# Optimization experiments

Hardware: AMD Instinct MI355X
Metric: run time of the kernel (lower is better)

Reference implementation:

```python
import jax, jax.numpy as jnp
import numpy as np
import math

B, T, D, H, DM = 2, 2048, 1024, 16, 256
DK = D // H

def setup_inputs() -> dict:
    key = jax.random.key(0)
    ks = jax.random.split(key, 13)
    s = 0.02
    return {
        "Hx": jax.random.normal(ks[0], (B, D, T, 1), jnp.float32),
        "Hf": jax.random.normal(ks[1], (B, T, D), jnp.float32),
        "Gm": jax.random.normal(ks[2], (B, T, DM), jnp.float32),
        "Wg": jax.random.normal(ks[3], (T, DM), jnp.float32) * s,
        "bg": jax.random.normal(ks[4], (T,), jnp.float32) * s,
        "Wq": jax.random.normal(ks[5], (D, 2 * D), jnp.float32) * s,
        "bq": jax.random.normal(ks[6], (D,), jnp.float32) * s,
        "Wk": jax.random.normal(ks[7], (D, 2 * D), jnp.float32) * s,
        "bk": jax.random.normal(ks[8], (D,), jnp.float32) * s,
        "Wv": jax.random.normal(ks[9], (D, D), jnp.float32) * s,
        "bv": jax.random.normal(ks[10], (D,), jnp.float32) * s,
        "Wo": jax.random.normal(ks[11], (D, D), jnp.float32) * s,
        "bo": jax.random.normal(ks[12], (D,), jnp.float32) * s,
    }

def reference(Hx, Hf, Gm, Wg, bg, Wq, bq, Wk, bk, Wv, bv, Wo, bo):
    # Hx: (B, D, T, 1) -> (B, T, D)
    hx = jnp.transpose(Hx[..., 0], (0, 2, 1))
    h_cat = jnp.concatenate([hx, Hf], axis=-1)          # (B, T, 2D)
    Q = h_cat @ Wq.T + bq                               # (B, T, D)
    K = h_cat @ Wk.T + bk
    V = hx @ Wv.T + bv
    # split heads: (B, H, T, DK)
    Q = Q.reshape(B, T, H, DK).transpose(0, 2, 1, 3)
    K = K.reshape(B, T, H, DK).transpose(0, 2, 1, 3)
    V = V.reshape(B, T, H, DK).transpose(0, 2, 1, 3)
    scores = jnp.einsum('bhqd,bhkd->bhqk', Q, K) / math.sqrt(DK)
    bias = Gm @ Wg.T + bg                                # (B, T, T)
    scores = scores + bias[:, None, :, :]
    attn = jax.nn.softmax(scores, axis=-1)
    out = jnp.einsum('bhqk,bhkd->bhqd', attn, V)
    out = out.transpose(0, 2, 1, 3).reshape(B, T, D)
    return out @ Wo.T + bo
```

## Files before the change

kernel.cpp:

```cpp
#include <hip/hip_runtime.h>
#include <hip/hip_bf16.h>

using bf16 = __hip_bfloat16;
typedef __attribute__((ext_vector_type(8))) __bf16 bf16x8;
typedef __attribute__((ext_vector_type(4))) float f32x4;

#define GLB_AS(p) ((const __attribute__((address_space(1))) unsigned int*)(p))
#define LDS_AS(p) ((__attribute__((address_space(3))) unsigned int*)(p))

__device__ __forceinline__ void async_copy16(const void* g, void* l) {
  __builtin_amdgcn_global_load_lds(GLB_AS(g), LDS_AS(l), 16, 0, 0);
}

__device__ __forceinline__ f32x4 mfma16x16x32(bf16x8 a, bf16x8 b, f32x4 c) {
  return __builtin_amdgcn_mfma_f32_16x16x32_bf16(a, b, c, 0, 0, 0);
}

__device__ __forceinline__ float bfu2f(unsigned short u) {
  union { unsigned int i; float f; } x;
  x.i = (unsigned int)u << 16;
  return x.f;
}

#define LOG2E 1.44269504f

__global__ __launch_bounds__(256) void pack_hx(const float* __restrict__ Hx,
                                               bf16* __restrict__ hcat) {
  __shared__ float tile[64][65];
  const int t0 = blockIdx.x * 64, d0 = blockIdx.y * 64, b = blockIdx.z;
  const int c = threadIdx.x & 63, r0 = threadIdx.x >> 6;
#pragma unroll
  for (int i = 0; i < 16; ++i) {
    const int rd = r0 + i * 4;
    tile[rd][c] = Hx[((size_t)(b * 1024 + d0 + rd)) * 2048 + t0 + c];
  }
  __syncthreads();
#pragma unroll
  for (int i = 0; i < 16; ++i) {
    const int ct = r0 + i * 4;
    hcat[((size_t)(b * 2048 + t0 + ct)) * 2048 + d0 + c] =
        __float2bfloat16(tile[c][ct]);
  }
}

__global__ __launch_bounds__(256) void pack_all(
    const float* __restrict__ Hf, const float* __restrict__ Wq,
    const float* __restrict__ Wk, const float* __restrict__ Wv,
    const float* __restrict__ Wo, const float* __restrict__ Wg,
    const float* __restrict__ Gm, const float* __restrict__ bq,
    const float* __restrict__ bk, const float* __restrict__ bv,
    bf16* __restrict__ hcat, bf16* __restrict__ Wqkvb, bf16* __restrict__ Wob,
    bf16* __restrict__ Wgb, bf16* __restrict__ Gmb,
    float* __restrict__ qkvbias) {
  const int gid = blockIdx.x * 256 + threadIdx.x;
  const float* src = nullptr;
  bf16* dst = nullptr;
  int lg = 0, ldo = 0, off = 0, idx = 0;
  bool zero = false;
  if (gid < 1048576) { idx = gid; src = Hf; dst = hcat; lg = 8; ldo = 2048; off = 1024; }
  else if (gid < 1572864) { idx = gid - 1048576; src = Wq; dst = Wqkvb; lg = 9; ldo = 2048; }
  else if (gid < 2097152) { idx = gid - 1572864; src = Wk; dst = Wqkvb + (size_t)1024 * 2048; lg = 9; ldo = 2048; }
  else if (gid < 2359296) { idx = gid - 2097152; src = Wv; dst = Wqkvb + (size_t)2048 * 2048; lg = 8; ldo = 2048; }
  else if (gid < 2621440) { idx = gid - 2359296; zero = true; dst = Wqkvb + (size_t)2048 * 2048 + 1024; lg = 8; ldo = 2048; }
  else if (gid < 2883584) { idx = gid - 2621440; src = Wo; dst = Wob; lg = 8; ldo = 1024; }
  else if (gid < 3014656) { idx = gid - 2883584; src = Wg; dst = Wgb; lg = 6; ldo = 256; }
  else if (gid < 3276800) { idx = gid - 3014656; src = Gm; dst = Gmb; lg = 6; ldo = 256; }
  else if (gid < 3277056) { const int i = gid - 3276800; ((float4*)qkvbias)[i] = ((const float4*)bq)[i]; return; }
  else if (gid < 3277312) { const int i = gid - 3277056; ((float4*)(qkvbias + 1024))[i] = ((const float4*)bk)[i]; return; }
  else { const int i = gid - 3277312; ((float4*)(qkvbias + 2048))[i] = ((const float4*)bv)[i]; return; }
  const int row = idx >> lg, c = idx & ((1 << lg) - 1);
  bf16* o = dst + (size_t)row * ldo + off + c * 4;
  __align__(8) bf16 tmp[4];
  if (zero) {
    tmp[0] = tmp[1] = tmp[2] = tmp[3] = __float2bfloat16(0.f);
  } else {
    const float4 v = ((const float4*)src)[(size_t)idx];
    tmp[0] = __float2bfloat16(v.x); tmp[1] = __float2bfloat16(v.y);
    tmp[2] = __float2bfloat16(v.z); tmp[3] = __float2bfloat16(v.w);
  }
  *(ushort4*)o = *(const ushort4*)tmp;
}

__global__ __launch_bounds__(512, 2) void gemm_qkv_bias(
    const bf16* __restrict__ hcat, const bf16* __restrict__ Wqkv,
    const float* __restrict__ qkvbias, const bf16* __restrict__ Gmb,
    const bf16* __restrict__ Wgb, const float* __restrict__ bg,
    bf16* __restrict__ QKb, bf16* __restrict__ Vt, bf16* __restrict__ biasS) {
  __shared__ __align__(16) bf16 AS[2][256][64];
  __shared__ __align__(16) bf16 BS[2][256][64];
  const int lin = blockIdx.x;
  const bool isqkv = lin < 192;
  int m0, n0, Kd, KT, nit2;
  const bf16 *Ag, *Bg;
  const float* biasv;
  if (isqkv) {
    const int xcd = lin & 7, kk = lin >> 3;
    const int mloc = kk / 6, nloc = kk - mloc * 6;
    m0 = ((xcd >> 1) * 4 + mloc) * 256;
    n0 = ((xcd & 1) * 6 + nloc) * 256;
    Ag = hcat; Bg = Wqkv; biasv = qkvbias;
    Kd = 2048; KT = 32; nit2 = 16;
  } else {
    const int l2 = lin - 192;
    m0 = (l2 >> 3) * 256;
    n0 = (l2 & 7) * 256;
    Ag = Gmb; Bg = Wgb; biasv = bg;
    Kd = 256; KT = 4; nit2 = 2;
  }
  const int tid = threadIdx.x, lane = tid & 63, w = tid >> 6;
  const int w8 = w * 8, ln3 = lane >> 3, ch = lane & 7;
  const int fr = lane & 15, ck = lane >> 4;
  const int wm64 = (w >> 2) * 64;
  const int wn32 = (w & 3) * 32;

  f32x4 acc[8][4];
  const f32x4 fzero = {0.f, 0.f, 0.f, 0.f};
#pragma unroll
  for (int i = 0; i < 8; ++i)
#pragma unroll
    for (int j = 0; j < 4; ++j) acc[i][j] = fzero;

  auto stageA = [&](int buf, int mh, int kt) {
    const int k0 = kt * 64;
#pragma unroll
    for (int l = 0; l < 2; ++l) {
      const int rit = mh * 128 + l * 64 + w8 + ln3;
      async_copy16(Ag + (size_t)(m0 + rit) * Kd + k0 + ((ch ^ ln3) << 3),
                   (char*)&AS[buf][0][0] + ((mh * 128 + l * 64 + w8) << 7));
    }
  };
  auto stageB = [&](int buf, int nh, int kt) {
    const int k0 = kt * 64;
#pragma unroll
    for (int l = 0; l < 2; ++l) {
      const int rit = nh * 128 + l * 64 + w8 + ln3;
      async_copy16(Bg + (size_t)(n0 + rit) * Kd + k0 + ((ch ^ ln3) << 3),
                   (char*)&BS[buf][0][0] + ((nh * 128 + l * 64 + w8) << 7));
    }
  };

  bf16x8 af[4][2], bA[2][2], bB[2][2];
  auto ldA = [&](int buf, int mh) {
#pragma unroll
    for (int i = 0; i < 4; ++i)
#pragma unroll
      for (int ks = 0; ks < 2; ++ks)
        af[i][ks] = *(const bf16x8*)(
            &AS[buf][mh * 128 + wm64 + i * 16 + fr][0] +
            (((ks * 4 + ck) ^ (fr & 7)) << 3));
  };
  auto ldB = [&](bf16x8 (&dst)[2][2], int buf, int nh) {
#pragma unroll
    for (int j = 0; j < 2; ++j)
#pragma unroll
      for (int ks = 0; ks < 2; ++ks)
        dst[j][ks] = *(const bf16x8*)(
            &BS[buf][nh * 128 + wn32 + j * 16 + fr][0] +
            (((ks * 4 + ck) ^ (fr & 7)) << 3));
  };

#define BAR() __builtin_amdgcn_s_barrier()
#define LGKM0() asm volatile("s_waitcnt lgkmcnt(0)" ::: "memory")
#define MMAQ(MH, NH, BF)                                                      \
  __builtin_amdgcn_s_setprio(1);                                              \
  _Pragma("unroll") for (int i_ = 0; i_ < 4; ++i_) {                          \
    _Pragma("unroll") for (int j_ = 0; j_ < 2; ++j_) {                        \
      acc[(MH) * 4 + i_][(NH) * 2 + j_] = mfma16x16x32(                       \
          af[i_][0], BF[j_][0], acc[(MH) * 4 + i_][(NH) * 2 + j_]);           \
      acc[(MH) * 4 + i_][(NH) * 2 + j_] = mfma16x16x32(                       \
          af[i_][1], BF[j_][1], acc[(MH) * 4 + i_][(NH) * 2 + j_]);           \
    }                                                                         \
  }                                                                           \
  __builtin_amdgcn_s_setprio(0);

  stageA(0, 0, 0); stageB(0, 0, 0); stageB(0, 1, 0); stageA(0, 1, 0);
  stageA(1, 0, 1); stageB(1, 0, 1);
  asm volatile("s_waitcnt vmcnt(4)" ::: "memory");
  BAR();

  for (int it = 0; it < nit2; ++it) {
    const int kodd = 2 * it + 1;
    const int kn0 = (2 * it + 2 < KT) ? 2 * it + 2 : KT - 1;
    const int kn1 = (2 * it + 3 < KT) ? 2 * it + 3 : KT - 1;

    ldA(0, 0); ldB(bA, 0, 0);
    stageB(1, 1, kodd);
    asm volatile("s_waitcnt lgkmcnt(8)");
    BAR(); LGKM0();
    MMAQ(0, 0, bA);
    BAR();
    ldB(bB, 0, 1);
    stageA(1, 1, kodd);
    BAR(); LGKM0();
    MMAQ(0, 1, bB);
    BAR();
    ldA(0, 1);
    stageA(0, 0, kn0);
    BAR(); LGKM0();
    MMAQ(1, 0, bA);
    BAR();
    stageB(0, 0, kn0);
    asm volatile("s_waitcnt vmcnt(4)" ::: "memory");
    BAR();
    MMAQ(1, 1, bB);
    BAR();
    ldA(1, 0); ldB(bA, 1, 0);
    stageB(0, 1, kn0);
    asm volatile("s_waitcnt lgkmcnt(8)");
    BAR(); LGKM0();
    MMAQ(0, 0, bA);
    BAR();
    ldB(bB, 1, 1);
    stageA(0, 1, kn0);
    BAR(); LGKM0();
    MMAQ(0, 1, bB);
    BAR();
    ldA(1, 1);
    stageA(1, 0, kn1);
    BAR(); LGKM0();
    MMAQ(1, 0, bA);
    BAR();
    stageB(1, 0, kn1);
    asm volatile("s_waitcnt vmcnt(4)" ::: "memory");
    BAR();
    MMAQ(1, 1, bB);
    BAR();
  }
  asm volatile("s_waitcnt vmcnt(0)" ::: "memory");

  const int erow = (lane >> 4) * 4, ecol = lane & 15;
  if (!isqkv) {
#pragma unroll
    for (int ai = 0; ai < 8; ++ai) {
      const int gm0 = m0 + (ai >> 2) * 128 + wm64 + (ai & 3) * 16 + erow;
#pragma unroll
      for (int bj = 0; bj < 4; ++bj) {
        const int gn = n0 + (bj >> 1) * 128 + wn32 + (bj & 1) * 16 + ecol;
        const float bv = biasv[gn];
#pragma unroll
        for (int r = 0; r < 4; ++r)
          biasS[(size_t)(gm0 + r) * 2048 + gn] =
              __float2bfloat16((acc[ai][bj][r] + bv) * LOG2E);
      }
    }
  } else if (n0 < 2048) {
    const float sc = (n0 < 1024) ? 0.125f * LOG2E : 1.0f;
#pragma unroll
    for (int ai = 0; ai < 8; ++ai) {
      const int gm0 = m0 + (ai >> 2) * 128 + wm64 + (ai & 3) * 16 + erow;
#pragma unroll
      for (int bj = 0; bj < 4; ++bj) {
        const int gn = n0 + (bj >> 1) * 128 + wn32 + (bj & 1) * 16 + ecol;
        const float bv = biasv[gn];
#pragma unroll
        for (int r = 0; r < 4; ++r)
          QKb[(size_t)(gm0 + r) * 2048 + gn] =
              __float2bfloat16((acc[ai][bj][r] + bv) * sc);
      }
    }
  } else {
#pragma unroll
    for (int ai = 0; ai < 8; ++ai) {
      const int gm0 = m0 + (ai >> 2) * 128 + wm64 + (ai & 3) * 16 + erow;
      const int bb = gm0 >> 11;
      const int t = gm0 & 2047;
#pragma unroll
      for (int bj = 0; bj < 4; ++bj) {
        const int gn = n0 + (bj >> 1) * 128 + wn32 + (bj & 1) * 16 + ecol;
        const float bv = biasv[gn];
        const int d = gn - 2048;
        __align__(8) bf16 tmp[4];
#pragma unroll
        for (int r = 0; r < 4; ++r)
          tmp[r] = __float2bfloat16(acc[ai][bj][r] + bv);
        *(ushort4*)(Vt + ((size_t)(bb * 1024 + d)) * 2048 + t) =
            *(const ushort4*)tmp;
      }
    }
  }
#undef MMAQ
#undef LGKM0
#undef BAR
}

__global__ __launch_bounds__(256) void gemm_out(const bf16* __restrict__ A,
                                                const bf16* __restrict__ W,
                                                const float* __restrict__ biasv,
                                                float* __restrict__ C) {
  __shared__ __align__(16) bf16 As[2][128 * 64];
  __shared__ __align__(16) bf16 Bs[2][64 * 64];
  const int lin = blockIdx.x;
  const int xcd = lin & 7;
  const int kk = lin >> 3;
  const int m0 = (kk >> 1) * 128;
  const int n0 = (xcd * 2 + (kk & 1)) * 64;
  const int tid = threadIdx.x, lane = tid & 63, w = tid >> 6;
  const int wm = (w >> 1) * 64, wn = (w & 1) * 32;
  const int fr = lane & 15;
  const int ck = lane >> 4;

  f32x4 acc[4][2];
  const f32x4 fzero = {0.f, 0.f, 0.f, 0.f};
#pragma unroll
  for (int i = 0; i < 4; ++i)
#pragma unroll
    for (int j = 0; j < 2; ++j) acc[i][j] = fzero;

  auto stage = [&](int it, int buf) {
    const int k0 = it * 64;
#pragma unroll
    for (int is = 0; is < 4; ++is) {
      const int off = is * 4096 + w * 1024;
      const int row = (off >> 7) + (lane >> 3);
      const int sch = ((lane & 7) ^ (row & 7)) * 8;
      async_copy16(A + (size_t)(m0 + row) * 1024 + k0 + sch,
                   (char*)As[buf] + off);
      if (is < 2)
        async_copy16(W + (size_t)(n0 + row) * 1024 + k0 + sch,
                     (char*)Bs[buf] + off);
    }
  };

  stage(0, 0);
  __syncthreads();
  for (int it = 0; it < 16; ++it) {
    const int cur = it & 1;
    if (it + 1 < 16) stage(it + 1, cur ^ 1);
#pragma unroll
    for (int ks = 0; ks < 2; ++ks) {
      bf16x8 af[4], bfr[2];
      const int swk0 = (((ks * 4 + ck) ^ (fr & 7))) * 8;
#pragma unroll
      for (int i = 0; i < 4; ++i)
        af[i] = *(const bf16x8*)(As[cur] + (wm + i * 16 + fr) * 64 + swk0);
#pragma unroll
      for (int j = 0; j < 2; ++j)
        bfr[j] = *(const bf16x8*)(Bs[cur] + (wn + j * 16 + fr) * 64 + swk0);
#pragma unroll
      for (int i = 0; i < 4; ++i)
#pragma unroll
        for (int j = 0; j < 2; ++j)
          acc[i][j] = mfma16x16x32(af[i], bfr[j], acc[i][j]);
    }
    __syncthreads();
  }
  const int erow = (lane >> 4) * 4;
  const int ecol = lane & 15;
#pragma unroll
  for (int i = 0; i < 4; ++i) {
    const int gm0 = m0 + wm + i * 16 + erow;
#pragma unroll
    for (int j = 0; j < 2; ++j) {
      const int gn = n0 + wn + j * 16 + ecol;
      const float bv = biasv[gn];
#pragma unroll
      for (int r = 0; r < 4; ++r)
        C[(size_t)(gm0 + r) * 1024 + gn] = acc[i][j][r] + bv;
    }
  }
}

__global__ __launch_bounds__(256) void flash_attn(
    const bf16* __restrict__ Qm, const bf16* __restrict__ Km,
    const bf16* __restrict__ Vtm, const bf16* __restrict__ biasS,
    float* __restrict__ Op0, float* __restrict__ Op1,
    float* __restrict__ lpart) {
  __shared__ __align__(16) bf16 Ks[2][64 * 64];
  __shared__ __align__(16) bf16 Vs[2][64 * 64];
  __shared__ __align__(16) bf16 Ps[4 * 32 * 72];
  const int lin = blockIdx.x;
  const int xcd = lin & 7;
  const int kk = lin >> 3;
  const int cl = kk & 1;
  const int r2 = kk >> 1;
  const int half = r2 & 1;
  const int q0 = (r2 >> 1) * 128;
  const int combo = xcd * 2 + cl;
  const int hp = combo & 7;
  const int b = combo >> 3;
  const int tid = threadIdx.x, lane = tid & 63, w = tid >> 6;
  const int ql = lane & 15, qk = lane >> 4;
  const int T = 2048, D = 1024;
  const int sw0 = (qk ^ (ql & 7)) * 8;
  const int sw1 = ((qk + 4) ^ (ql & 7)) * 8;

  bf16x8 qf[2][2][2];
#pragma unroll
  for (int hh = 0; hh < 2; ++hh)
#pragma unroll
    for (int qt = 0; qt < 2; ++qt)
#pragma unroll
      for (int ks = 0; ks < 2; ++ks)
        qf[hh][qt][ks] = *(const bf16x8*)(
            Qm + (size_t)(b * T + q0 + w * 32 + qt * 16 + ql) * 2048 +
            (hp * 2 + hh) * 64 + ks * 32 + qk * 8);

  f32x4 acc[2][4][2];
  const f32x4 fzero = {0.f, 0.f, 0.f, 0.f};
#pragma unroll
  for (int hh = 0; hh < 2; ++hh)
#pragma unroll
    for (int dt = 0; dt < 4; ++dt)
#pragma unroll
      for (int qt = 0; qt < 2; ++qt) acc[hh][dt][qt] = fzero;
  float lp[2][2] = {{0.f, 0.f}, {0.f, 0.f}};

  const bf16* kbase0 = Km + (size_t)(b * T) * 2048 + (hp * 2) * 64;
  const bf16* vbase0 = Vtm + (size_t)(b * D + hp * 2 * 64) * 2048;
  const bf16* bb0 = biasS + (size_t)(b * T + q0 + w * 32 + ql) * 2048 + qk * 4;
  bf16* pb = Ps + w * 2304;

  for (int j = 0; j < 16; ++j) {
    const int jj = half * 16 + j;
    __syncthreads();
#pragma unroll
    for (int hh = 0; hh < 2; ++hh)
#pragma unroll
      for (int is = 0; is < 2; ++is) {
        const int off = is * 4096 + w * 1024;
        const int row = (off >> 7) + (lane >> 3);
        const int sch = ((lane & 7) ^ (row & 7)) * 8;
        async_copy16(kbase0 + (size_t)(jj * 64 + row) * 2048 + hh * 64 + sch,
                     (char*)Ks[hh] + off);
        async_copy16(vbase0 + (size_t)(hh * 64 + row) * 2048 + jj * 64 + sch,
                     (char*)Vs[hh] + off);
      }
    ushort4 bq[2][4];
#pragma unroll
    for (int qt = 0; qt < 2; ++qt)
#pragma unroll
      for (int jt = 0; jt < 4; ++jt)
        bq[qt][jt] = *(const ushort4*)(bb0 + (size_t)qt * 16 * 2048 + jj * 64 +
                                       jt * 16);
    __syncthreads();
#pragma unroll
    for (int hh = 0; hh < 2; ++hh) {
      const bf16* ksp = Ks[hh];
      const bf16* vsp = Vs[hh];
#pragma unroll
      for (int jt = 0; jt < 4; ++jt) {
        const bf16x8 kf0 = *(const bf16x8*)(ksp + (jt * 16 + ql) * 64 + sw0);
        const bf16x8 kf1 = *(const bf16x8*)(ksp + (jt * 16 + ql) * 64 + sw1);
#pragma unroll
        for (int qt = 0; qt < 2; ++qt) {
          f32x4 c;
          c[0] = bfu2f(bq[qt][jt].x); c[1] = bfu2f(bq[qt][jt].y);
          c[2] = bfu2f(bq[qt][jt].z); c[3] = bfu2f(bq[qt][jt].w);
          c = mfma16x16x32(kf0, qf[hh][qt][0], c);
          c = mfma16x16x32(kf1, qf[hh][qt][1], c);
          __align__(8) bf16 t4[4];
#pragma unroll
          for (int r = 0; r < 4; ++r) {
            const float pv = __builtin_amdgcn_exp2f(c[r]);
            lp[hh][qt] += pv;
            t4[r] = __float2bfloat16(pv);
          }
          *(ushort4*)(pb + (qt * 16 + ql) * 72 + jt * 16 + qk * 4) =
              *(const ushort4*)t4;
        }
      }
#pragma unroll
      for (int ks = 0; ks < 2; ++ks) {
        const bf16x8 pf0 = *(const bf16x8*)(pb + ql * 72 + ks * 32 + qk * 8);
        const bf16x8 pf1 =
            *(const bf16x8*)(pb + (16 + ql) * 72 + ks * 32 + qk * 8);
        const int sw = ks ? sw1 : sw0;
#pragma unroll
        for (int dt = 0; dt < 4; ++dt) {
          const bf16x8 vf = *(const bf16x8*)(vsp + (dt * 16 + ql) * 64 + sw);
          acc[hh][dt][0] = mfma16x16x32(pf0, vf, acc[hh][dt][0]);
          acc[hh][dt][1] = mfma16x16x32(pf1, vf, acc[hh][dt][1]);
        }
      }
    }
  }
#pragma unroll
  for (int hh = 0; hh < 2; ++hh)
#pragma unroll
    for (int qt = 0; qt < 2; ++qt) {
      lp[hh][qt] += __shfl_xor(lp[hh][qt], 16);
      lp[hh][qt] += __shfl_xor(lp[hh][qt], 32);
    }
  if (qk == 0) {
#pragma unroll
    for (int hh = 0; hh < 2; ++hh)
#pragma unroll
      for (int qt = 0; qt < 2; ++qt)
        lpart[half * 65536 + (b * 16 + hp * 2 + hh) * 2048 + q0 + w * 32 +
              qt * 16 + ql] = lp[hh][qt];
  }
  float* Op = half ? Op1 : Op0;
#pragma unroll
  for (int hh = 0; hh < 2; ++hh)
#pragma unroll
    for (int qt = 0; qt < 2; ++qt)
#pragma unroll
      for (int r = 0; r < 4; ++r) {
        const size_t orow =
            (size_t)(b * T + q0 + w * 32 + qt * 16 + qk * 4 + r);
#pragma unroll
        for (int dt = 0; dt < 4; ++dt)
          Op[orow * 1024 + (hp * 2 + hh) * 64 + dt * 16 + ql] =
              acc[hh][dt][qt][r];
      }
}

__global__ __launch_bounds__(256) void combine(const float* __restrict__ O0,
                                               const float* __restrict__ O1,
                                               const float* __restrict__ lpart,
                                               bf16* __restrict__ AOut) {
  const int idx = blockIdx.x * 256 + threadIdx.x;
  const int row = idx >> 8;
  const int col = (idx & 255) * 4;
  const int b = row >> 11, q = row & 2047, h = col >> 6;
  const int li = (b * 16 + h) * 2048 + q;
  const float inv = __builtin_amdgcn_rcpf(lpart[li] + lpart[65536 + li]);
  const float4 a = *(const float4*)(O0 + (size_t)row * 1024 + col);
  const float4 c = *(const float4*)(O1 + (size_t)row * 1024 + col);
  __align__(8) bf16 t[4] = {
      __float2bfloat16((a.x + c.x) * inv), __float2bfloat16((a.y + c.y) * inv),
      __float2bfloat16((a.z + c.z) * inv), __float2bfloat16((a.w + c.w) * inv)};
  *(ushort4*)(AOut + (size_t)row * 1024 + col) = *(const ushort4*)t;
}

extern "C" void kernel_launch(void* const* d_in, const int* in_sizes, int n_in,
                              void* d_out, int out_size, void* d_ws,
                              size_t ws_size, hipStream_t stream) {
  (void)in_sizes; (void)n_in; (void)out_size; (void)ws_size;
  const float* Hx = (const float*)d_in[0];
  const float* Hf = (const float*)d_in[1];
  const float* Gm = (const float*)d_in[2];
  const float* Wg = (const float*)d_in[3];
  const float* bg = (const float*)d_in[4];
  const float* Wq = (const float*)d_in[5];
  const float* bq = (const float*)d_in[6];
  const float* Wk = (const float*)d_in[7];
  const float* bk = (const float*)d_in[8];
  const float* Wv = (const float*)d_in[9];
  const float* bv = (const float*)d_in[10];
  const float* Wo = (const float*)d_in[11];
  const float* bo = (const float*)d_in[12];
  float* out = (float*)d_out;

  char* p = (char*)d_ws;
  bf16* hcat = (bf16*)p;   p += (size_t)4096 * 2048 * 2;
  bf16* QKb = (bf16*)p;    p += (size_t)4096 * 2048 * 2;
  bf16* Vtb = (bf16*)p;    p += (size_t)4096 * 1024 * 2;
  bf16* biasS = (bf16*)p;  p += (size_t)4096 * 2048 * 2;
  bf16* AOut = (bf16*)p;   p += (size_t)4096 * 1024 * 2;
  bf16* Wqkvb = (bf16*)p;  p += (size_t)3072 * 2048 * 2;
  bf16* Wob = (bf16*)p;    p += (size_t)1024 * 1024 * 2;
  bf16* Wgb = (bf16*)p;    p += (size_t)2048 * 256 * 2;
  bf16* Gmb = (bf16*)p;    p += (size_t)4096 * 256 * 2;
  float* qkvbias = (float*)p; p += (size_t)3072 * 4;
  float* Op1 = (float*)p;  p += (size_t)4096 * 1024 * 4;
  float* lpart = (float*)p; p += (size_t)2 * 65536 * 4;
  float* Op0 = (float*)hcat;

  pack_hx<<<dim3(32, 16, 2), 256, 0, stream>>>(Hx, hcat);
  pack_all<<<dim3(12803), 256, 0, stream>>>(Hf, Wq, Wk, Wv, Wo, Wg, Gm, bq, bk,
                                            bv, hcat, Wqkvb, Wob, Wgb, Gmb,
                                            qkvbias);
  gemm_qkv_bias<<<dim3(320), 512, 0, stream>>>(hcat, Wqkvb, qkvbias, Gmb,
                                               Wgb, bg, QKb, Vtb, biasS);
  flash_attn<<<dim3(512), 256, 0, stream>>>(QKb, QKb + 1024, Vtb, biasS,
                                            Op0, Op1, lpart);
  combine<<<dim3(4096), 256, 0, stream>>>(Op0, Op1, lpart, AOut);
  gemm_out<<<dim3(512), 256, 0, stream>>>(AOut, Wob, bo, out);
}
```

Baseline: 278.2 us.

## Double-buffer K/V tiles and prefetch bias one iteration ahead in attention

Result: slower. 346.3 us (+24.5%).

```diff
diff --git a/kernel.cpp b/kernel.cpp
--- a/kernel.cpp
+++ b/kernel.cpp
@@ -383,6 +383,8 @@
   const int T = 2048, D = 1024;
   const int sw0 = (qk ^ (ql & 7)) * 8;
   const int sw1 = ((qk + 4) ^ (ql & 7)) * 8;
+  const int ln3 = lane >> 3;
+  const int sch = ((lane & 7) ^ ln3) << 3;
 
   bf16x8 qf[2][2][2];
 #pragma unroll
@@ -410,70 +412,110 @@
   const bf16* bb0 = biasS + (size_t)(b * T + q0 + w * 32 + ql) * 2048 + qk * 4;
   bf16* pb = Ps + w * 2304;
 
-  for (int j = 0; j < 16; ++j) {
-    const int jj = half * 16 + j;
-    __syncthreads();
-#pragma unroll
-    for (int hh = 0; hh < 2; ++hh)
-#pragma unroll
-      for (int is = 0; is < 2; ++is) {
-        const int off = is * 4096 + w * 1024;
-        const int row = (off >> 7) + (lane >> 3);
-        const int sch = ((lane & 7) ^ (row & 7)) * 8;
-        async_copy16(kbase0 + (size_t)(jj * 64 + row) * 2048 + hh * 64 + sch,
-                     (char*)Ks[hh] + off);
-        async_copy16(vbase0 + (size_t)(hh * 64 + row) * 2048 + jj * 64 + sch,
-                     (char*)Vs[hh] + off);
+  ushort4 bqA[2][4], bqB[2][4];
+
+  {
+    const int jj0 = half * 16;
+#pragma unroll
+    for (int is = 0; is < 2; ++is) {
+      const int off = is * 4096 + w * 1024;
+      const int row = is * 32 + w * 8 + ln3;
+      async_copy16(kbase0 + (size_t)(jj0 * 64 + row) * 2048 + sch,
+                   (char*)Ks[0] + off);
+      async_copy16(vbase0 + (size_t)row * 2048 + jj0 * 64 + sch,
+                   (char*)Vs[0] + off);
+    }
+#pragma unroll
+    for (int qt = 0; qt < 2; ++qt)
+#pragma unroll
+      for (int jt = 0; jt < 4; ++jt)
+        bqA[qt][jt] = *(const ushort4*)(bb0 + (size_t)qt * 16 * 2048 +
+                                        jj0 * 64 + jt * 16);
+  }
+
+#define AITER(HH, CUR, BQC, BQN, NHV, NJV)                                     \
+  {                                                                            \
+    const int nh_ = (NHV);                                                     \
+    const int njj_ = half * 16 + (NJV);                                        \
+    _Pragma("unroll") for (int is_ = 0; is_ < 2; ++is_) {                      \
+      const int off_ = is_ * 4096 + w * 1024;                                  \
+      const int row_ = is_ * 32 + w * 8 + ln3;                                 \
+      async_copy16(                                                            \
+          kbase0 + (size_t)(njj_ * 64 + row_) * 2048 + nh_ * 64 + sch,         \
+          (char*)Ks[(CUR) ^ 1] + off_);                                        \
+      async_copy16(                                                            \
+          vbase0 + (size_t)(nh_ * 64 + row_) * 2048 + njj_ * 64 + sch,         \
+          (char*)Vs[(CUR) ^ 1] + off_);                                        \
+    }                                                                          \
+    _Pragma("unroll") for (int qt_ = 0; qt_ < 2; ++qt_)                        \
+        _Pragma("unroll") for (int jt_ = 0; jt_ < 4; ++jt_)                    \
+            BQN[qt_][jt_] = *(const ushort4*)(bb0 + (size_t)qt_ * 16 * 2048 +  \
+                                              njj_ * 64 + jt_ * 16);           \
+    asm volatile("s_waitcnt vmcnt(12)" ::: "memory");                          \
+    __builtin_amdgcn_s_barrier();                                              \
+    {                                                                          \
+      const bf16* ksp_ = Ks[CUR];                                              \
+      const bf16* vsp_ = Vs[CUR];                                              \
+      _Pragma("unroll") for (int jt_ = 0; jt_ < 4; ++jt_) {                    \
+        const bf16x8 kf0_ =                                                    \
+            *(const bf16x8*)(ksp_ + (jt_ * 16 + ql) * 64 + sw0);               \
+        const bf16x8 kf1_ =                                                    \
+            *(const bf16x8*)(ksp_ + (jt_ * 16 + ql) * 64 + sw1);               \
+        _Pragma("unroll") for (int qt_ = 0; qt_ < 2; ++qt_) {                  \
+          f32x4 c_;                                                            \
+          c_[0] = bfu2f(BQC[qt_][jt_].x);                                      \
+          c_[1] = bfu2f(BQC[qt_][jt_].y);                                      \
+          c_[2] = bfu2f(BQC[qt_][jt_].z);                                      \
+          c_[3] = bfu2f(BQC[qt_][jt_].w);                                      \
+          c_ = mfma16x16x32(kf0_, qf[HH][qt_][0], c_);                         \
+          c_ = mfma16x16x32(kf1_, qf[HH][qt_][1], c_);                         \
+          __align__(8) bf16 t4_[4];                                            \
+          _Pragma("unroll") for (int r_ = 0; r_ < 4; ++r_) {                   \
+            const float pv_ = __builtin_amdgcn_exp2f(c_[r_]);                  \
+            lp[HH][qt_] += pv_;                                                \
+            t4_[r_] = __float2bfloat16(pv_);                                   \
+          }                                                                    \
+          *(ushort4*)(pb + (qt_ * 16 + ql) * 72 + jt_ * 16 + qk * 4) =         \
+              *(const ushort4*)t4_;                                            \
+        }                                                                      \
+      }                                                                        \
+      __builtin_amdgcn_s_setprio(1);                                           \
+      _Pragma("unroll") for (int ks_ = 0; ks_ < 2; ++ks_) {                    \
+        const bf16x8 pf0_ =                                                    \
+            *(const bf16x8*)(pb + ql * 72 + ks_ * 32 + qk * 8);                \
+        const bf16x8 pf1_ =                                                    \
+            *(const bf16x8*)(pb + (16 + ql) * 72 + ks_ * 32 + qk * 8);         \
+        const int sw_ = ks_ ? sw1 : sw0;                                       \
+        _Pragma("unroll") for (int dt_ = 0; dt_ < 4; ++dt_) {                  \
+          const bf16x8 vf_ =                                                   \
+              *(const bf16x8*)(vsp_ + (dt_ * 16 + ql) * 64 + sw_);             \
+          acc[HH][dt_][0] = mfma16x16x32(pf0_, vf_, acc[HH][dt_][0]);          \
+          acc[HH][dt_][1] = mfma16x16x32(pf1_, vf_, acc[HH][dt_][1]);          \
+        }                                                                      \
+      }                                                                        \
+      __builtin_amdgcn_s_setprio(0);                                           \
+    }                                                                          \
+    __builtin_amdgcn_s_barrier();                                              \
+  }
+
+#pragma unroll
+  for (int hh = 0; hh < 2; ++hh) {
+    for (int jp = 0; jp < 8; ++jp) {
+      {
+        const int nj = jp * 2 + 1;
+        AITER(hh, 0, bqA, bqB, hh, nj)
       }
-    ushort4 bq[2][4];
-#pragma unroll
-    for (int qt = 0; qt < 2; ++qt)
-#pragma unroll
-      for (int jt = 0; jt < 4; ++jt)
-        bq[qt][jt] = *(const ushort4*)(bb0 + (size_t)qt * 16 * 2048 + jj * 64 +
-                                       jt * 16);
-    __syncthreads();
-#pragma unroll
-    for (int hh = 0; hh < 2; ++hh) {
-      const bf16* ksp = Ks[hh];
-      const bf16* vsp = Vs[hh];
-#pragma unroll
-      for (int jt = 0; jt < 4; ++jt) {
-        const bf16x8 kf0 = *(const bf16x8*)(ksp + (jt * 16 + ql) * 64 + sw0);
-        const bf16x8 kf1 = *(const bf16x8*)(ksp + (jt * 16 + ql) * 64 + sw1);
-#pragma unroll
-        for (int qt = 0; qt < 2; ++qt) {
-          f32x4 c;
-          c[0] = bfu2f(bq[qt][jt].x); c[1] = bfu2f(bq[qt][jt].y);
-          c[2] = bfu2f(bq[qt][jt].z); c[3] = bfu2f(bq[qt][jt].w);
-          c = mfma16x16x32(kf0, qf[hh][qt][0], c);
-          c = mfma16x16x32(kf1, qf[hh][qt][1], c);
-          __align__(8) bf16 t4[4];
-#pragma unroll
-          for (int r = 0; r < 4; ++r) {
-            const float pv = __builtin_amdgcn_exp2f(c[r]);
-            lp[hh][qt] += pv;
-            t4[r] = __float2bfloat16(pv);
-          }
-          *(ushort4*)(pb + (qt * 16 + ql) * 72 + jt * 16 + qk * 4) =
-              *(const ushort4*)t4;
-        }
+      {
+        int nh = hh, nj = jp * 2 + 2;
+        if (nj == 16) { nh = hh + 1; nj = 0; }
+        if (nh == 2) { nh = 1; nj = 15; }
+        AITER(hh, 1, bqB, bqA, nh, nj)
       }
-#pragma unroll
-      for (int ks = 0; ks < 2; ++ks) {
-        const bf16x8 pf0 = *(const bf16x8*)(pb + ql * 72 + ks * 32 + qk * 8);
-        const bf16x8 pf1 =
-            *(const bf16x8*)(pb + (16 + ql) * 72 + ks * 32 + qk * 8);
-        const int sw = ks ? sw1 : sw0;
-#pragma unroll
-        for (int dt = 0; dt < 4; ++dt) {
-          const bf16x8 vf = *(const bf16x8*)(vsp + (dt * 16 + ql) * 64 + sw);
-          acc[hh][dt][0] = mfma16x16x32(pf0, vf, acc[hh][dt][0]);
-          acc[hh][dt][1] = mfma16x16x32(pf1, vf, acc[hh][dt][1]);
-        }
-      }
-    }
-  }
+    }
+  }
+#undef AITER
+  asm volatile("s_waitcnt vmcnt(0)" ::: "memory");
+
 #pragma unroll
   for (int hh = 0; hh < 2; ++hh)
 #pragma unroll
```

## Split flash attention blocks to one head each and raise PV MFMA priority

Applied to the files above, without the earlier changes.

New measurement: 304.6 us. 9.5% more time.

```diff
diff --git a/kernel.cpp b/kernel.cpp
--- a/kernel.cpp
+++ b/kernel.cpp
@@ -365,48 +365,41 @@
     const bf16* __restrict__ Vtm, const bf16* __restrict__ biasS,
     float* __restrict__ Op0, float* __restrict__ Op1,
     float* __restrict__ lpart) {
-  __shared__ __align__(16) bf16 Ks[2][64 * 64];
-  __shared__ __align__(16) bf16 Vs[2][64 * 64];
+  __shared__ __align__(16) bf16 Ks[64 * 64];
+  __shared__ __align__(16) bf16 Vs[64 * 64];
   __shared__ __align__(16) bf16 Ps[4 * 32 * 72];
   const int lin = blockIdx.x;
-  const int xcd = lin & 7;
-  const int kk = lin >> 3;
-  const int cl = kk & 1;
-  const int r2 = kk >> 1;
-  const int half = r2 & 1;
-  const int q0 = (r2 >> 1) * 128;
-  const int combo = xcd * 2 + cl;
-  const int hp = combo & 7;
-  const int b = combo >> 3;
+  const int h = lin >> 6;
+  const int g = lin & 63;
+  const int qblk = g >> 2;
+  const int half = (g >> 1) & 1;
+  const int b = g & 1;
+  const int q0 = qblk * 128;
   const int tid = threadIdx.x, lane = tid & 63, w = tid >> 6;
   const int ql = lane & 15, qk = lane >> 4;
   const int T = 2048, D = 1024;
   const int sw0 = (qk ^ (ql & 7)) * 8;
   const int sw1 = ((qk + 4) ^ (ql & 7)) * 8;
 
-  bf16x8 qf[2][2][2];
-#pragma unroll
-  for (int hh = 0; hh < 2; ++hh)
-#pragma unroll
-    for (int qt = 0; qt < 2; ++qt)
-#pragma unroll
-      for (int ks = 0; ks < 2; ++ks)
-        qf[hh][qt][ks] = *(const bf16x8*)(
-            Qm + (size_t)(b * T + q0 + w * 32 + qt * 16 + ql) * 2048 +
-            (hp * 2 + hh) * 64 + ks * 32 + qk * 8);
-
-  f32x4 acc[2][4][2];
+  bf16x8 qf[2][2];
+#pragma unroll
+  for (int qt = 0; qt < 2; ++qt)
+#pragma unroll
+    for (int ks = 0; ks < 2; ++ks)
+      qf[qt][ks] = *(const bf16x8*)(
+          Qm + (size_t)(b * T + q0 + w * 32 + qt * 16 + ql) * 2048 + h * 64 +
+          ks * 32 + qk * 8);
+
+  f32x4 acc[4][2];
   const f32x4 fzero = {0.f, 0.f, 0.f, 0.f};
 #pragma unroll
-  for (int hh = 0; hh < 2; ++hh)
-#pragma unroll
-    for (int dt = 0; dt < 4; ++dt)
-#pragma unroll
-      for (int qt = 0; qt < 2; ++qt) acc[hh][dt][qt] = fzero;
-  float lp[2][2] = {{0.f, 0.f}, {0.f, 0.f}};
-
-  const bf16* kbase0 = Km + (size_t)(b * T) * 2048 + (hp * 2) * 64;
-  const bf16* vbase0 = Vtm + (size_t)(b * D + hp * 2 * 64) * 2048;
+  for (int dt = 0; dt < 4; ++dt)
+#pragma unroll
+    for (int qt = 0; qt < 2; ++qt) acc[dt][qt] = fzero;
+  float lp[2] = {0.f, 0.f};
+
+  const bf16* kbase = Km + (size_t)(b * T) * 2048 + h * 64;
+  const bf16* vbase = Vtm + (size_t)(b * D + h * 64) * 2048;
   const bf16* bb0 = biasS + (size_t)(b * T + q0 + w * 32 + ql) * 2048 + qk * 4;
   bf16* pb = Ps + w * 2304;
 
@@ -414,17 +407,15 @@
     const int jj = half * 16 + j;
     __syncthreads();
 #pragma unroll
-    for (int hh = 0; hh < 2; ++hh)
-#pragma unroll
-      for (int is = 0; is < 2; ++is) {
-        const int off = is * 4096 + w * 1024;
-        const int row = (off >> 7) + (lane >> 3);
-        const int sch = ((lane & 7) ^ (row & 7)) * 8;
-        async_copy16(kbase0 + (size_t)(jj * 64 + row) * 2048 + hh * 64 + sch,
-                     (char*)Ks[hh] + off);
-        async_copy16(vbase0 + (size_t)(hh * 64 + row) * 2048 + jj * 64 + sch,
-                     (char*)Vs[hh] + off);
-      }
+    for (int is = 0; is < 2; ++is) {
+      const int off = is * 4096 + w * 1024;
+      const int row = (off >> 7) + (lane >> 3);
+      const int sch = ((lane & 7) ^ (row & 7)) * 8;
+      async_copy16(kbase + (size_t)(jj * 64 + row) * 2048 + sch,
+                   (char*)Ks + off);
+      async_copy16(vbase + (size_t)row * 2048 + jj * 64 + sch,
+                   (char*)Vs + off);
+    }
     ushort4 bq[2][4];
 #pragma unroll
     for (int qt = 0; qt < 2; ++qt)
@@ -434,75 +425,64 @@
                                        jt * 16);
     __syncthreads();
 #pragma unroll
-    for (int hh = 0; hh < 2; ++hh) {
-      const bf16* ksp = Ks[hh];
-      const bf16* vsp = Vs[hh];
-#pragma unroll
-      for (int jt = 0; jt < 4; ++jt) {
-        const bf16x8 kf0 = *(const bf16x8*)(ksp + (jt * 16 + ql) * 64 + sw0);
-        const bf16x8 kf1 = *(const bf16x8*)(ksp + (jt * 16 + ql) * 64 + sw1);
-#pragma unroll
-        for (int qt = 0; qt < 2; ++qt) {
-          f32x4 c;
-          c[0] = bfu2f(bq[qt][jt].x); c[1] = bfu2f(bq[qt][jt].y);
-          c[2] = bfu2f(bq[qt][jt].z); c[3] = bfu2f(bq[qt][jt].w);
-          c = mfma16x16x32(kf0, qf[hh][qt][0], c);
-          c = mfma16x16x32(kf1, qf[hh][qt][1], c);
-          __align__(8) bf16 t4[4];
-#pragma unroll
-          for (int r = 0; r < 4; ++r) {
-            const float pv = __builtin_amdgcn_exp2f(c[r]);
-            lp[hh][qt] += pv;
-            t4[r] = __float2bfloat16(pv);
-          }
-          *(ushort4*)(pb + (qt * 16 + ql) * 72 + jt * 16 + qk * 4) =
-              *(const ushort4*)t4;
+    for (int jt = 0; jt < 4; ++jt) {
+      const bf16x8 kf0 = *(const bf16x8*)(Ks + (jt * 16 + ql) * 64 + sw0);
+      const bf16x8 kf1 = *(const bf16x8*)(Ks + (jt * 16 + ql) * 64 + sw1);
+#pragma unroll
+      for (int qt = 0; qt < 2; ++qt) {
+        f32x4 c;
+        c[0] = bfu2f(bq[qt][jt].x); c[1] = bfu2f(bq[qt][jt].y);
+        c[2] = bfu2f(bq[qt][jt].z); c[3] = bfu2f(bq[qt][jt].w);
+        c = mfma16x16x32(kf0, qf[qt][0], c);
+        c = mfma16x16x32(kf1, qf[qt][1], c);
+        __align__(8) bf16 t4[4];
+#pragma unroll
+        for (int r = 0; r < 4; ++r) {
+          const float pv = __builtin_amdgcn_exp2f(c[r]);
+          lp[qt] += pv;
+          t4[r] = __float2bfloat16(pv);
         }
+        *(ushort4*)(pb + (qt * 16 + ql) * 72 + jt * 16 + qk * 4) =
+            *(const ushort4*)t4;
       }
-#pragma unroll
-      for (int ks = 0; ks < 2; ++ks) {
-        const bf16x8 pf0 = *(const bf16x8*)(pb + ql * 72 + ks * 32 + qk * 8);
-        const bf16x8 pf1 =
-            *(const bf16x8*)(pb + (16 + ql) * 72 + ks * 32 + qk * 8);
-        const int sw = ks ? sw1 : sw0;
-#pragma unroll
-        for (int dt = 0; dt < 4; ++dt) {
-          const bf16x8 vf = *(const bf16x8*)(vsp + (dt * 16 + ql) * 64 + sw);
-          acc[hh][dt][0] = mfma16x16x32(pf0, vf, acc[hh][dt][0]);
-          acc[hh][dt][1] = mfma16x16x32(pf1, vf, acc[hh][dt][1]);
-        }
+    }
+    __builtin_amdgcn_s_setprio(1);
+#pragma unroll
+    for (int ks = 0; ks < 2; ++ks) {
+      const bf16x8 pf0 = *(const bf16x8*)(pb + ql * 72 + ks * 32 + qk * 8);
+      const bf16x8 pf1 =
+          *(const bf16x8*)(pb + (16 + ql) * 72 + ks * 32 + qk * 8);
+      const int sw = ks ? sw1 : sw0;
+#pragma unroll
+      for (int dt = 0; dt < 4; ++dt) {
+        const bf16x8 vf = *(const bf16x8*)(Vs + (dt * 16 + ql) * 64 + sw);
+        acc[dt][0] = mfma16x16x32(pf0, vf, acc[dt][0]);
+        acc[dt][1] = mfma16x16x32(pf1, vf, acc[dt][1]);
       }
     }
-  }
-#pragma unroll
-  for (int hh = 0; hh < 2; ++hh)
-#pragma unroll
-    for (int qt = 0; qt < 2; ++qt) {
-      lp[hh][qt] += __shfl_xor(lp[hh][qt], 16);
-      lp[hh][qt] += __shfl_xor(lp[hh][qt], 32);
-    }
+    __builtin_amdgcn_s_setprio(0);
+  }
+#pragma unroll
+  for (int qt = 0; qt < 2; ++qt) {
+    lp[qt] += __shfl_xor(lp[qt], 16);
+    lp[qt] += __shfl_xor(lp[qt], 32);
+  }
   if (qk == 0) {
 #pragma unroll
-    for (int hh = 0; hh < 2; ++hh)
-#pragma unroll
-      for (int qt = 0; qt < 2; ++qt)
-        lpart[half * 65536 + (b * 16 + hp * 2 + hh) * 2048 + q0 + w * 32 +
-              qt * 16 + ql] = lp[hh][qt];
+    for (int qt = 0; qt < 2; ++qt)
+      lpart[half * 65536 + (b * 16 + h) * 2048 + q0 + w * 32 + qt * 16 + ql] =
+          lp[qt];
   }
   float* Op = half ? Op1 : Op0;
 #pragma unroll
-  for (int hh = 0; hh < 2; ++hh)
-#pragma unroll
-    for (int qt = 0; qt < 2; ++qt)
-#pragma unroll
-      for (int r = 0; r < 4; ++r) {
-        const size_t orow =
-            (size_t)(b * T + q0 + w * 32 + qt * 16 + qk * 4 + r);
-#pragma unroll
-        for (int dt = 0; dt < 4; ++dt)
-          Op[orow * 1024 + (hp * 2 + hh) * 64 + dt * 16 + ql] =
-              acc[hh][dt][qt][r];
-      }
+  for (int qt = 0; qt < 2; ++qt)
+#pragma unroll
+    for (int r = 0; r < 4; ++r) {
+      const size_t orow = (size_t)(b * T + q0 + w * 32 + qt * 16 + qk * 4 + r);
+#pragma unroll
+      for (int dt = 0; dt < 4; ++dt)
+        Op[orow * 1024 + h * 64 + dt * 16 + ql] = acc[dt][qt][r];
+    }
 }
 
 __global__ __launch_bounds__(256) void combine(const float* __restrict__ O0,
@@ -563,8 +543,8 @@
                                             qkvbias);
   gemm_qkv_bias<<<dim3(320), 512, 0, stream>>>(hcat, Wqkvb, qkvbias, Gmb,
                                                Wgb, bg, QKb, Vtb, biasS);
-  flash_attn<<<dim3(512), 256, 0, stream>>>(QKb, QKb + 1024, Vtb, biasS,
-                                            Op0, Op1, lpart);
+  flash_attn<<<dim3(1024), 256, 0, stream>>>(QKb, QKb + 1024, Vtb, biasS,
+                                             Op0, Op1, lpart);
   combine<<<dim3(4096), 256, 0, stream>>>(Op0, Op1, lpart, AOut);
   gemm_out<<<dim3(512), 256, 0, stream>>>(AOut, Wob, bo, out);
 }
```
